# Kernel optimization log

Measured on AMD Instinct MI355X. Metric: run time of the kernel, lower is better.

Reference implementation:

```python
import jax, jax.numpy as jnp
import numpy as np
import math

B, S, D, H = 4, 2048, 1024, 16
HD = D // H  # head_dim = 64


def setup_inputs() -> dict:
    key = jax.random.key(0)
    ks = jax.random.split(key, 7)
    s = 0.02
    return {
        "q": jax.random.normal(ks[0], (B, S, D), jnp.float32),
        "k": jax.random.normal(ks[1], (B, S, D), jnp.float32),
        "v": jax.random.normal(ks[2], (B, S, D), jnp.float32),
        "wq": jax.random.normal(ks[3], (D, D), jnp.float32) * s,
        "wk": jax.random.normal(ks[4], (D, D), jnp.float32) * s,
        "wv": jax.random.normal(ks[5], (D, D), jnp.float32) * s,
        "wo": jax.random.normal(ks[6], (D, D), jnp.float32) * s,
    }


def reference(q, k, v, wq, wk, wv, wo):
    # Linear (no bias): y = x @ W.T, W is (out, in)
    xq = jnp.einsum('bsd,ed->bse', q, wq).reshape(B, S, H, HD).transpose(0, 2, 1, 3)
    xk = jnp.einsum('bsd,ed->bse', k, wk).reshape(B, S, H, HD).transpose(0, 2, 1, 3)
    xv = jnp.einsum('bsd,ed->bse', v, wv).reshape(B, S, H, HD).transpose(0, 2, 1, 3)
    scores = jnp.einsum('bhqd,bhkd->bhqk', xq, xk) / math.sqrt(HD)  # [B,H,S,S]
    causal = jnp.tril(jnp.ones((S, S), dtype=bool))
    scores = jnp.where(causal[None, None], scores, jnp.float32(-jnp.inf))
    probs = jax.nn.softmax(scores, axis=-1)  # dropout p=0 -> identity
    out = jnp.einsum('bhqk,bhkd->bhqd', probs, xv)  # [B,H,S,HD]
    out = out.transpose(0, 2, 1, 3).reshape(B, S, D)
    return jnp.einsum('bsd,ed->bse', out, wo)
```

## Files before the change

kernel.cpp:

```cpp
#include <hip/hip_runtime.h>

#define SS 2048
#define DD 1024
#define HH 16
#define HD 64
#define MM 8192

typedef unsigned short ushort_t;
typedef __attribute__((ext_vector_type(8))) short short8;
typedef __attribute__((ext_vector_type(4))) float f32x4;
typedef __attribute__((ext_vector_type(4))) unsigned short us4;
typedef __attribute__((ext_vector_type(8))) unsigned short us8;

__device__ __forceinline__ ushort_t f2bf(float f) {
    union { float f; unsigned u; } x; x.f = f;
    unsigned r = x.u + 0x7fffu + ((x.u >> 16) & 1u);
    return (ushort_t)(r >> 16);
}
__device__ __forceinline__ float bf2f(ushort_t h) {
    union { unsigned u; float f; } x; x.u = ((unsigned)h) << 16; return x.f;
}
__device__ __forceinline__ unsigned pack_bf2(float a, float b) {
    union { float f; unsigned u; } x, y; x.f = a; y.f = b;
    return __builtin_amdgcn_perm(y.u, x.u, 0x07060302u);
}

__device__ __forceinline__ void async16(const void* g, void* l) {
    __builtin_amdgcn_global_load_lds(
        (const __attribute__((address_space(1))) unsigned int*)g,
        (__attribute__((address_space(3))) unsigned int*)l, 16, 0, 0);
}

__global__ void cvt_all(const float* __restrict__ q, const float* __restrict__ k,
                        const float* __restrict__ v, const float* __restrict__ wq,
                        const float* __restrict__ wk, const float* __restrict__ wv,
                        const float* __restrict__ wo, ushort_t* __restrict__ qbf,
                        ushort_t* __restrict__ kbf, ushort_t* __restrict__ vbf,
                        ushort_t* __restrict__ wbf) {
    long i = ((long)blockIdx.x * 256 + threadIdx.x) * 8;
    const float* src; ushort_t* dst;
    if (i < (3l << 23)) {
        int s = (int)(i >> 23);
        long off = i & ((1l << 23) - 1);
        src = ((s == 0) ? q : (s == 1) ? k : v) + off;
        dst = ((s == 0) ? qbf : (s == 1) ? kbf : vbf) + off;
    } else {
        long j = i - (3l << 23);
        int s = (int)(j >> 20);
        src = ((s == 0) ? wq : (s == 1) ? wk : (s == 2) ? wv : wo) + (j & 1048575);
        dst = wbf + j;
    }
    float4 f0 = *(const float4*)src;
    float4 f1 = *(const float4*)(src + 4);
    us8 o;
    o[0] = f2bf(f0.x); o[1] = f2bf(f0.y); o[2] = f2bf(f0.z); o[3] = f2bf(f0.w);
    o[4] = f2bf(f1.x); o[5] = f2bf(f1.y); o[6] = f2bf(f1.z); o[7] = f2bf(f1.w);
    *(us8*)dst = o;
}

__device__ __forceinline__ void epi_scatter(f32x4 acc[4][4], int m0, int n0,
                                            int mode, void* Yv) {
    int tid = threadIdx.x;
    int w = tid >> 6, lane = tid & 63;
    int l16 = lane & 15, quad = lane >> 4;
    int wm = (w >> 1) * 64, wn = (w & 1) * 64;
    #pragma unroll
    for (int mt = 0; mt < 4; ++mt) {
        #pragma unroll
        for (int r = 0; r < 4; ++r) {
            int row = m0 + wm + mt * 16 + quad * 4 + r;
            #pragma unroll
            for (int nt = 0; nt < 4; ++nt) {
                int col = n0 + wn + nt * 16 + l16;
                float vf = acc[mt][nt][r];
                if (mode == 2) {
                    ((float*)Yv)[(size_t)row * DD + col] = vf;
                } else {
                    ushort_t vh = f2bf(vf);
                    int b = row >> 11, s = row & 2047;
                    int h = col >> 6,  hd = col & 63;
                    if (mode == 0) {
                        ((ushort_t*)Yv)[(((size_t)b * HH + h) * SS + s) * HD + hd] = vh;
                    } else {
                        int sp = (s & ~63) | (((s & 15) << 2) | ((s >> 4) & 3));
                        ((ushort_t*)Yv)[(((size_t)b * HH + h) * HD + hd) * SS + sp] = vh;
                    }
                }
            }
        }
    }
}

__global__ __launch_bounds__(256) void proj3f(const ushort_t* __restrict__ qbf,
                                              const ushort_t* __restrict__ kbf,
                                              const ushort_t* __restrict__ vbf,
                                              const ushort_t* __restrict__ Wall,
                                              ushort_t* __restrict__ xq,
                                              ushort_t* __restrict__ xk,
                                              ushort_t* __restrict__ xvT) {
    __shared__ __align__(16) ushort_t As[3][128 * 32];
    __shared__ __align__(16) ushort_t Bs[3][128 * 32];
    int tid = threadIdx.x;
    int w = tid >> 6, lane = tid & 63;
    int l16 = lane & 15, quad = lane >> 4;
    int mat   = (int)(blockIdx.x >> 9);
    int inner = (int)(blockIdx.x & 511);
    int m0 = (inner & 63) * 128;
    int n0 = (inner >> 6) * 128;
    const ushort_t* A  = (mat == 0) ? qbf : (mat == 1) ? kbf : vbf;
    const ushort_t* Bw = Wall + ((size_t)mat << 20);
    int wm = (w >> 1) * 64, wn = (w & 1) * 64;

    f32x4 acc[4][4];
    #pragma unroll
    for (int i = 0; i < 4; ++i)
        #pragma unroll
        for (int j = 0; j < 4; ++j) acc[i][j] = (f32x4){0.f, 0.f, 0.f, 0.f};

    int g0 = w * 64 + lane, r0 = g0 >> 2, j0 = ((g0 & 3) ^ (r0 & 3)) * 8;
    int g1 = g0 + 256,      r1 = g1 >> 2, j1 = ((g1 & 3) ^ (r1 & 3)) * 8;
    int swA = (quad ^ (l16 & 3)) * 8;

    const ushort_t* Ar0 = A  + (size_t)(m0 + r0) * DD + j0;
    const ushort_t* Ar1 = A  + (size_t)(m0 + r1) * DD + j1;
    const ushort_t* Br0 = Bw + (size_t)(n0 + r0) * DD + j0;
    const ushort_t* Br1 = Bw + (size_t)(n0 + r1) * DD + j1;
    int ldsA0 = w * 64 * 8, ldsA1 = (256 + w * 64) * 8;

    async16(Ar0,      &As[0][ldsA0]);
    async16(Ar1,      &As[0][ldsA1]);
    async16(Br0,      &Bs[0][ldsA0]);
    async16(Br1,      &Bs[0][ldsA1]);
    async16(Ar0 + 32, &As[1][ldsA0]);
    async16(Ar1 + 32, &As[1][ldsA1]);
    async16(Br0 + 32, &Bs[1][ldsA0]);
    async16(Br1 + 32, &Bs[1][ldsA1]);

    int c = 0, c2 = 2;
    for (int kk = 0; kk < 32; ++kk) {
        __builtin_amdgcn_s_barrier();
        if (kk < 30) {
            int k2 = (kk + 2) * 32;
            async16(Ar0 + k2, &As[c2][ldsA0]);
            async16(Ar1 + k2, &As[c2][ldsA1]);
            async16(Br0 + k2, &Bs[c2][ldsA0]);
            async16(Br1 + k2, &Bs[c2][ldsA1]);
            asm volatile("s_waitcnt vmcnt(8)" ::: "memory");
        } else if (kk == 30) {
            asm volatile("s_waitcnt vmcnt(4)" ::: "memory");
        } else {
            asm volatile("s_waitcnt vmcnt(0)" ::: "memory");
        }
        __builtin_amdgcn_s_barrier();
        __builtin_amdgcn_sched_barrier(0);

        short8 af[4], bfr[4];
        #pragma unroll
        for (int t = 0; t < 4; ++t) {
            af[t]  = *(const short8*)&As[c][(wm + t * 16 + l16) * 32 + swA];
            bfr[t] = *(const short8*)&Bs[c][(wn + t * 16 + l16) * 32 + swA];
        }
        #pragma unroll
        for (int mt = 0; mt < 4; ++mt)
            #pragma unroll
            for (int nt = 0; nt < 4; ++nt)
                acc[mt][nt] = __builtin_amdgcn_mfma_f32_16x16x32_bf16(af[mt], bfr[nt], acc[mt][nt], 0, 0, 0);

        c  = (c  == 2) ? 0 : c  + 1;
        c2 = (c2 == 2) ? 0 : c2 + 1;
    }

    void* Y = (mat == 0) ? (void*)xq : (mat == 1) ? (void*)xk : (void*)xvT;
    epi_scatter(acc, m0, n0, (mat == 2) ? 1 : 0, Y);
}

__global__ __launch_bounds__(512) void out_gemm(const ushort_t* __restrict__ Abf,
                                                const ushort_t* __restrict__ Bw,
                                                float* __restrict__ Y) {
    __shared__ __align__(16) ushort_t As[2][256 * 32];
    __shared__ __align__(16) ushort_t Bs[2][128 * 32];
    int tid = threadIdx.x;
    int w = tid >> 6, lane = tid & 63;
    int l16 = lane & 15, quad = lane >> 4;
    int inner = (int)blockIdx.x;
    int m0 = (inner & 31) * 256;
    int n0 = (inner >> 5) * 128;
    int wm = (w >> 1) * 64, wn = (w & 1) * 64;

    f32x4 acc[4][4];
    #pragma unroll
    for (int i = 0; i < 4; ++i)
        #pragma unroll
        for (int j = 0; j < 4; ++j) acc[i][j] = (f32x4){0.f, 0.f, 0.f, 0.f};

    int ra0 = tid >> 2,           ja0 = ((tid & 3) ^ (ra0 & 3)) * 8;
    int ga1 = tid + 512;
    int ra1 = ga1 >> 2,           ja1 = ((ga1 & 3) ^ (ra1 & 3)) * 8;
    int rb  = tid >> 2,           jb  = ((tid & 3) ^ (rb & 3)) * 8;
    int swA = (quad ^ (l16 & 3)) * 8;

    async16(Abf + (size_t)(m0 + ra0) * DD + ja0, &As[0][(size_t)(w * 64) * 8]);
    async16(Abf + (size_t)(m0 + ra1) * DD + ja1, &As[0][(size_t)(512 + w * 64) * 8]);
    async16(Bw  + (size_t)(n0 + rb)  * DD + jb,  &Bs[0][(size_t)(w * 64) * 8]);

    for (int kk = 0; kk < 32; ++kk) {
        int c = kk & 1;
        __syncthreads();
        if (kk < 31) {
            int k1 = (kk + 1) * 32;
            async16(Abf + (size_t)(m0 + ra0) * DD + k1 + ja0, &As[c ^ 1][(size_t)(w * 64) * 8]);
            async16(Abf + (size_t)(m0 + ra1) * DD + k1 + ja1, &As[c ^ 1][(size_t)(512 + w * 64) * 8]);
            async16(Bw  + (size_t)(n0 + rb)  * DD + k1 + jb,  &Bs[c ^ 1][(size_t)(w * 64) * 8]);
        }
        short8 af[4], bfr[4];
        #pragma unroll
        for (int t = 0; t < 4; ++t) {
            af[t]  = *(const short8*)&As[c][(wm + t * 16 + l16) * 32 + swA];
            bfr[t] = *(const short8*)&Bs[c][(wn + t * 16 + l16) * 32 + swA];
        }
        #pragma unroll
        for (int mt = 0; mt < 4; ++mt)
            #pragma unroll
            for (int nt = 0; nt < 4; ++nt)
                acc[mt][nt] = __builtin_amdgcn_mfma_f32_16x16x32_bf16(af[mt], bfr[nt], acc[mt][nt], 0, 0, 0);
    }
    epi_scatter(acc, m0, n0, 2, Y);
}

__global__ __launch_bounds__(256) void attn_kernel(const ushort_t* __restrict__ xq,
                                                   const ushort_t* __restrict__ xk,
                                                   const ushort_t* __restrict__ xvT,
                                                   ushort_t* __restrict__ ao) {
    __shared__ __align__(16) ushort_t Ksm[2][64 * 64];
    __shared__ __align__(16) ushort_t Vsm[2][64 * 64];
    __shared__ __align__(16) ushort_t Psm[4][16 * 72];

    int tid = threadIdx.x;
    int w = tid >> 6, lane = tid & 63;
    int l16 = lane & 15, quad = lane >> 4;
    int bh = blockIdx.x & 63;
    int p  = blockIdx.x >> 6;
    int b = bh >> 4, h = bh & 15;

    const ushort_t* Q  = xq  + (size_t)bh * SS * HD;
    const ushort_t* K  = xk  + (size_t)bh * SS * HD;
    const ushort_t* VT = xvT + (size_t)bh * HD * SS;

    int g0 = w * 64 + lane, r0 = g0 >> 3, j0 = ((g0 & 7) ^ (r0 & 7)) * 8;
    int g1 = g0 + 256,      r1 = g1 >> 3, j1 = ((g1 & 7) ^ (r1 & 7)) * 8;

    short8 ones;
    #pragma unroll
    for (int i = 0; i < 8; ++i) ones[i] = (short)0x3F80;

    const float CS = 0.125f * 1.44269504f;

    for (int ph = 0; ph < 2; ++ph) {
        int qt = ph ? (31 - p) : p;
        int qb = qt * 64;
        int qmin = qb + w * 16;

        short8 aq[2];
        #pragma unroll
        for (int kc = 0; kc < 2; ++kc) {
            short8 t = *(const short8*)(Q + (size_t)(qmin + l16) * HD + kc * 32 + quad * 8);
            #pragma unroll
            for (int i = 0; i < 8; ++i)
                t[i] = (short)f2bf(bf2f((ushort_t)t[i]) * CS);
            aq[kc] = t;
        }

        f32x4 o[4];
        #pragma unroll
        for (int dt = 0; dt < 4; ++dt) o[dt] = (f32x4){0.f, 0.f, 0.f, 0.f};
        f32x4 lacc = (f32x4){0.f, 0.f, 0.f, 0.f};

        __syncthreads();
        async16(K  + (size_t)r0 * HD + j0, &Ksm[0][(size_t)(w * 64) * 8]);
        async16(K  + (size_t)r1 * HD + j1, &Ksm[0][(size_t)(256 + w * 64) * 8]);
        async16(VT + (size_t)r0 * SS + j0, &Vsm[0][(size_t)(w * 64) * 8]);
        async16(VT + (size_t)r1 * SS + j1, &Vsm[0][(size_t)(256 + w * 64) * 8]);

        for (int kt = 0; kt <= qt; ++kt) {
            int kb = kt * 64;
            int c = kt & 1;
            __syncthreads();
            if (kt < qt) {
                int kb1 = kb + 64;
                async16(K  + (size_t)(kb1 + r0) * HD + j0, &Ksm[c ^ 1][(size_t)(w * 64) * 8]);
                async16(K  + (size_t)(kb1 + r1) * HD + j1, &Ksm[c ^ 1][(size_t)(256 + w * 64) * 8]);
                async16(VT + (size_t)r0 * SS + kb1 + j0, &Vsm[c ^ 1][(size_t)(w * 64) * 8]);
                async16(VT + (size_t)r1 * SS + kb1 + j1, &Vsm[c ^ 1][(size_t)(256 + w * 64) * 8]);
            }

            f32x4 sc[4];
            __builtin_amdgcn_s_setprio(1);
            #pragma unroll
            for (int nt = 0; nt < 4; ++nt) {
                int row = nt * 16 + l16;
                short8 bk0 = *(const short8*)&Ksm[c][row * 64 + ((0 + quad) ^ (l16 & 7)) * 8];
                short8 bk1 = *(const short8*)&Ksm[c][row * 64 + ((4 + quad) ^ (l16 & 7)) * 8];
                f32x4 cc = (f32x4){0.f, 0.f, 0.f, 0.f};
                cc = __builtin_amdgcn_mfma_f32_16x16x32_bf16(aq[0], bk0, cc, 0, 0, 0);
                cc = __builtin_amdgcn_mfma_f32_16x16x32_bf16(aq[1], bk1, cc, 0, 0, 0);
                sc[nt] = cc;
            }
            __builtin_amdgcn_s_setprio(0);

            bool msk = (kt == qt);
            #pragma unroll
            for (int r = 0; r < 4; ++r) {
                float e0, e1, e2, e3;
                if (msk) {
                    int qg = qmin + quad * 4 + r;
                    e0 = (kb +  0 + l16 <= qg) ? __builtin_amdgcn_exp2f(sc[0][r]) : 0.f;
                    e1 = (kb + 16 + l16 <= qg) ? __builtin_amdgcn_exp2f(sc[1][r]) : 0.f;
                    e2 = (kb + 32 + l16 <= qg) ? __builtin_amdgcn_exp2f(sc[2][r]) : 0.f;
                    e3 = (kb + 48 + l16 <= qg) ? __builtin_amdgcn_exp2f(sc[3][r]) : 0.f;
                } else {
                    e0 = __builtin_amdgcn_exp2f(sc[0][r]);
                    e1 = __builtin_amdgcn_exp2f(sc[1][r]);
                    e2 = __builtin_amdgcn_exp2f(sc[2][r]);
                    e3 = __builtin_amdgcn_exp2f(sc[3][r]);
                }
                uint2 pk = { pack_bf2(e0, e1), pack_bf2(e2, e3) };
                *(uint2*)&Psm[w][(quad * 4 + r) * 72 + l16 * 4] = pk;
            }

            asm volatile("s_waitcnt lgkmcnt(0)" ::: "memory");

            __builtin_amdgcn_s_setprio(1);
            #pragma unroll
            for (int kc = 0; kc < 2; ++kc) {
                short8 ap = *(const short8*)&Psm[w][l16 * 72 + kc * 32 + quad * 8];
                lacc = __builtin_amdgcn_mfma_f32_16x16x32_bf16(ap, ones, lacc, 0, 0, 0);
                #pragma unroll
                for (int dt = 0; dt < 4; ++dt) {
                    int row = dt * 16 + l16;
                    short8 bv = *(const short8*)&Vsm[c][row * 64 + ((kc * 4 + quad) ^ (l16 & 7)) * 8];
                    o[dt] = __builtin_amdgcn_mfma_f32_16x16x32_bf16(ap, bv, o[dt], 0, 0, 0);
                }
            }
            __builtin_amdgcn_s_setprio(0);
        }

        #pragma unroll
        for (int r = 0; r < 4; ++r) {
            float inv = 1.0f / lacc[r];
            int qg = qmin + quad * 4 + r;
            #pragma unroll
            for (int dt = 0; dt < 4; ++dt)
                ao[((size_t)(b * SS + qg)) * DD + h * HD + dt * 16 + l16] = f2bf(o[dt][r] * inv);
        }
    }
}

extern "C" void kernel_launch(void* const* d_in, const int* in_sizes, int n_in,
                              void* d_out, int out_size, void* d_ws, size_t ws_size,
                              hipStream_t stream) {
    const float* q  = (const float*)d_in[0];
    const float* k  = (const float*)d_in[1];
    const float* v  = (const float*)d_in[2];
    const float* wq = (const float*)d_in[3];
    const float* wk = (const float*)d_in[4];
    const float* wv = (const float*)d_in[5];
    const float* wo = (const float*)d_in[6];
    float* out = (float*)d_out;

    ushort_t* wbf = (ushort_t*)d_ws;
    ushort_t* xq  = wbf + 4194304ull;
    ushort_t* xk  = xq  + 8388608ull;
    ushort_t* xvT = xk  + 8388608ull;
    ushort_t* ao  = xvT + 8388608ull;
    ushort_t* vbf = ao;
    ushort_t* qbf = (ushort_t*)d_out;
    ushort_t* kbf = qbf + 8388608ull;

    cvt_all<<<14336, 256, 0, stream>>>(q, k, v, wq, wk, wv, wo, qbf, kbf, vbf, wbf);
    proj3f<<<1536, 256, 0, stream>>>(qbf, kbf, vbf, wbf, xq, xk, xvT);
    attn_kernel<<<1024, 256, 0, stream>>>(xq, xk, xvT, ao);
    out_gemm<<<256, 512, 0, stream>>>(ao, wbf + 3145728ull, out);
}
```

Before: 343.5 us.

## Double query tile per block to reuse K/V tiles across two row groups

Each wave now handles 32 query rows (two 16-row groups) instead of 16, so a block covers a 128-row query tile and the grid is halved. K and V fragments are loaded from shared memory once per key tile and reused for both row groups, which halves K/V global and LDS traffic per query. Causal masking is now decided per row group, since the diagonal spans two key tiles. The cost is more registers per thread (which may lower occupancy) and fewer blocks to balance across CUs.

```diff
diff --git a/kernel.cpp b/kernel.cpp
--- a/kernel.cpp
+++ b/kernel.cpp
@@ -256,24 +256,31 @@
     const float CS = 0.125f * 1.44269504f;
 
     for (int ph = 0; ph < 2; ++ph) {
-        int qt = ph ? (31 - p) : p;
-        int qb = qt * 64;
-        int qmin = qb + w * 16;
-
-        short8 aq[2];
-        #pragma unroll
-        for (int kc = 0; kc < 2; ++kc) {
-            short8 t = *(const short8*)(Q + (size_t)(qmin + l16) * HD + kc * 32 + quad * 8);
-            #pragma unroll
-            for (int i = 0; i < 8; ++i)
-                t[i] = (short)f2bf(bf2f((ushort_t)t[i]) * CS);
-            aq[kc] = t;
-        }
-
-        f32x4 o[4];
-        #pragma unroll
-        for (int dt = 0; dt < 4; ++dt) o[dt] = (f32x4){0.f, 0.f, 0.f, 0.f};
-        f32x4 lacc = (f32x4){0.f, 0.f, 0.f, 0.f};
+        int qt = ph ? (15 - p) : p;
+        int qb = qt * 128;
+        int qm0 = qb + w * 32;
+        int ktmax = 2 * qt + 1;
+
+        short8 aq[2][2];
+        #pragma unroll
+        for (int gm = 0; gm < 2; ++gm)
+            #pragma unroll
+            for (int kc = 0; kc < 2; ++kc) {
+                short8 t = *(const short8*)(Q + (size_t)(qm0 + gm * 16 + l16) * HD + kc * 32 + quad * 8);
+                #pragma unroll
+                for (int i = 0; i < 8; ++i)
+                    t[i] = (short)f2bf(bf2f((ushort_t)t[i]) * CS);
+                aq[gm][kc] = t;
+            }
+
+        f32x4 o[2][4];
+        f32x4 lacc[2];
+        #pragma unroll
+        for (int gm = 0; gm < 2; ++gm) {
+            lacc[gm] = (f32x4){0.f, 0.f, 0.f, 0.f};
+            #pragma unroll
+            for (int dt = 0; dt < 4; ++dt) o[gm][dt] = (f32x4){0.f, 0.f, 0.f, 0.f};
+        }
 
         __syncthreads();
         async16(K  + (size_t)r0 * HD + j0, &Ksm[0][(size_t)(w * 64) * 8]);
@@ -281,11 +288,11 @@
         async16(VT + (size_t)r0 * SS + j0, &Vsm[0][(size_t)(w * 64) * 8]);
         async16(VT + (size_t)r1 * SS + j1, &Vsm[0][(size_t)(256 + w * 64) * 8]);
 
-        for (int kt = 0; kt <= qt; ++kt) {
+        for (int kt = 0; kt <= ktmax; ++kt) {
             int kb = kt * 64;
             int c = kt & 1;
             __syncthreads();
-            if (kt < qt) {
+            if (kt < ktmax) {
                 int kb1 = kb + 64;
                 async16(K  + (size_t)(kb1 + r0) * HD + j0, &Ksm[c ^ 1][(size_t)(w * 64) * 8]);
                 async16(K  + (size_t)(kb1 + r1) * HD + j1, &Ksm[c ^ 1][(size_t)(256 + w * 64) * 8]);
@@ -293,65 +300,84 @@
                 async16(VT + (size_t)r1 * SS + kb1 + j1, &Vsm[c ^ 1][(size_t)(256 + w * 64) * 8]);
             }
 
-            f32x4 sc[4];
-            __builtin_amdgcn_s_setprio(1);
+            short8 bk0[4], bk1[4];
             #pragma unroll
             for (int nt = 0; nt < 4; ++nt) {
                 int row = nt * 16 + l16;
-                short8 bk0 = *(const short8*)&Ksm[c][row * 64 + ((0 + quad) ^ (l16 & 7)) * 8];
-                short8 bk1 = *(const short8*)&Ksm[c][row * 64 + ((4 + quad) ^ (l16 & 7)) * 8];
-                f32x4 cc = (f32x4){0.f, 0.f, 0.f, 0.f};
-                cc = __builtin_amdgcn_mfma_f32_16x16x32_bf16(aq[0], bk0, cc, 0, 0, 0);
-                cc = __builtin_amdgcn_mfma_f32_16x16x32_bf16(aq[1], bk1, cc, 0, 0, 0);
-                sc[nt] = cc;
-            }
+                bk0[nt] = *(const short8*)&Ksm[c][row * 64 + ((0 + quad) ^ (l16 & 7)) * 8];
+                bk1[nt] = *(const short8*)&Ksm[c][row * 64 + ((4 + quad) ^ (l16 & 7)) * 8];
+            }
+
+            f32x4 sc[2][4];
+            __builtin_amdgcn_s_setprio(1);
+            #pragma unroll
+            for (int gm = 0; gm < 2; ++gm)
+                #pragma unroll
+                for (int nt = 0; nt < 4; ++nt) {
+                    f32x4 cc = (f32x4){0.f, 0.f, 0.f, 0.f};
+                    cc = __builtin_amdgcn_mfma_f32_16x16x32_bf16(aq[gm][0], bk0[nt], cc, 0, 0, 0);
+                    cc = __builtin_amdgcn_mfma_f32_16x16x32_bf16(aq[gm][1], bk1[nt], cc, 0, 0, 0);
+                    sc[gm][nt] = cc;
+                }
             __builtin_amdgcn_s_setprio(0);
 
-            bool msk = (kt == qt);
-            #pragma unroll
-            for (int r = 0; r < 4; ++r) {
-                float e0, e1, e2, e3;
-                if (msk) {
-                    int qg = qmin + quad * 4 + r;
-                    e0 = (kb +  0 + l16 <= qg) ? __builtin_amdgcn_exp2f(sc[0][r]) : 0.f;
-                    e1 = (kb + 16 + l16 <= qg) ? __builtin_amdgcn_exp2f(sc[1][r]) : 0.f;
-                    e2 = (kb + 32 + l16 <= qg) ? __builtin_amdgcn_exp2f(sc[2][r]) : 0.f;
-                    e3 = (kb + 48 + l16 <= qg) ? __builtin_amdgcn_exp2f(sc[3][r]) : 0.f;
-                } else {
-                    e0 = __builtin_amdgcn_exp2f(sc[0][r]);
-                    e1 = __builtin_amdgcn_exp2f(sc[1][r]);
-                    e2 = __builtin_amdgcn_exp2f(sc[2][r]);
-                    e3 = __builtin_amdgcn_exp2f(sc[3][r]);
-                }
-                uint2 pk = { pack_bf2(e0, e1), pack_bf2(e2, e3) };
-                *(uint2*)&Psm[w][(quad * 4 + r) * 72 + l16 * 4] = pk;
-            }
-
-            asm volatile("s_waitcnt lgkmcnt(0)" ::: "memory");
-
-            __builtin_amdgcn_s_setprio(1);
-            #pragma unroll
-            for (int kc = 0; kc < 2; ++kc) {
-                short8 ap = *(const short8*)&Psm[w][l16 * 72 + kc * 32 + quad * 8];
-                lacc = __builtin_amdgcn_mfma_f32_16x16x32_bf16(ap, ones, lacc, 0, 0, 0);
+            short8 bv[2][4];
+            #pragma unroll
+            for (int kc = 0; kc < 2; ++kc)
                 #pragma unroll
                 for (int dt = 0; dt < 4; ++dt) {
                     int row = dt * 16 + l16;
-                    short8 bv = *(const short8*)&Vsm[c][row * 64 + ((kc * 4 + quad) ^ (l16 & 7)) * 8];
-                    o[dt] = __builtin_amdgcn_mfma_f32_16x16x32_bf16(ap, bv, o[dt], 0, 0, 0);
+                    bv[kc][dt] = *(const short8*)&Vsm[c][row * 64 + ((kc * 4 + quad) ^ (l16 & 7)) * 8];
                 }
-            }
-            __builtin_amdgcn_s_setprio(0);
-        }
-
-        #pragma unroll
-        for (int r = 0; r < 4; ++r) {
-            float inv = 1.0f / lacc[r];
-            int qg = qmin + quad * 4 + r;
-            #pragma unroll
-            for (int dt = 0; dt < 4; ++dt)
-                ao[((size_t)(b * SS + qg)) * DD + h * HD + dt * 16 + l16] = f2bf(o[dt][r] * inv);
-        }
+
+            #pragma unroll
+            for (int gm = 0; gm < 2; ++gm) {
+                int qmin = qm0 + gm * 16;
+                bool msk = (kb + 63 > qmin);
+                #pragma unroll
+                for (int r = 0; r < 4; ++r) {
+                    float e0, e1, e2, e3;
+                    if (msk) {
+                        int qg = qmin + quad * 4 + r;
+                        e0 = (kb +  0 + l16 <= qg) ? __builtin_amdgcn_exp2f(sc[gm][0][r]) : 0.f;
+                        e1 = (kb + 16 + l16 <= qg) ? __builtin_amdgcn_exp2f(sc[gm][1][r]) : 0.f;
+                        e2 = (kb + 32 + l16 <= qg) ? __builtin_amdgcn_exp2f(sc[gm][2][r]) : 0.f;
+                        e3 = (kb + 48 + l16 <= qg) ? __builtin_amdgcn_exp2f(sc[gm][3][r]) : 0.f;
+                    } else {
+                        e0 = __builtin_amdgcn_exp2f(sc[gm][0][r]);
+                        e1 = __builtin_amdgcn_exp2f(sc[gm][1][r]);
+                        e2 = __builtin_amdgcn_exp2f(sc[gm][2][r]);
+                        e3 = __builtin_amdgcn_exp2f(sc[gm][3][r]);
+                    }
+                    uint2 pk = { pack_bf2(e0, e1), pack_bf2(e2, e3) };
+                    *(uint2*)&Psm[w][(quad * 4 + r) * 72 + l16 * 4] = pk;
+                }
+
+                asm volatile("s_waitcnt lgkmcnt(0)" ::: "memory");
+
+                __builtin_amdgcn_s_setprio(1);
+                #pragma unroll
+                for (int kc = 0; kc < 2; ++kc) {
+                    short8 ap = *(const short8*)&Psm[w][l16 * 72 + kc * 32 + quad * 8];
+                    lacc[gm] = __builtin_amdgcn_mfma_f32_16x16x32_bf16(ap, ones, lacc[gm], 0, 0, 0);
+                    #pragma unroll
+                    for (int dt = 0; dt < 4; ++dt)
+                        o[gm][dt] = __builtin_amdgcn_mfma_f32_16x16x32_bf16(ap, bv[kc][dt], o[gm][dt], 0, 0, 0);
+                }
+                __builtin_amdgcn_s_setprio(0);
+            }
+        }
+
+        #pragma unroll
+        for (int gm = 0; gm < 2; ++gm)
+            #pragma unroll
+            for (int r = 0; r < 4; ++r) {
+                float inv = 1.0f / lacc[gm][r];
+                int qg = qm0 + gm * 16 + quad * 4 + r;
+                #pragma unroll
+                for (int dt = 0; dt < 4; ++dt)
+                    ao[((size_t)(b * SS + qg)) * DD + h * HD + dt * 16 + l16] = f2bf(o[gm][dt][r] * inv);
+            }
     }
 }
 
@@ -378,6 +404,6 @@
 
     cvt_all<<<14336, 256, 0, stream>>>(q, k, v, wq, wk, wv, wo, qbf, kbf, vbf, wbf);
     proj3f<<<1536, 256, 0, stream>>>(qbf, kbf, vbf, wbf, xq, xk, xvT);
-    attn_kernel<<<1024, 256, 0, stream>>>(xq, xk, xvT, ao);
+    attn_kernel<<<512, 256, 0, stream>>>(xq, xk, xvT, ao);
     out_gemm<<<256, 512, 0, stream>>>(ao, wbf + 3145728ull, out);
 }
```

New measurement: 331.7 us. 3.4% less time.
